# Kernel tuning notes

Measured on AMD Instinct MI355X. Metric: run time of the kernel, lower is better.

Reference implementation:

```python
import jax, jax.numpy as jnp
import numpy as np

B, T, C, H = 8, 1024, 768, 12
HD = C // H  # 64, even for RoPE
ROPE_THETA = 10000.0


def precompute_freqs_cis(dim, end, theta=ROPE_THETA):
    # [end, dim//2, 2] with (cos, sin) in last axis
    freqs = 1.0 / theta ** (jnp.arange(0, dim // 2).astype(jnp.float32) / (dim // 2))
    t = jnp.arange(end)
    f = jnp.outer(t, freqs)
    return jnp.stack([jnp.cos(f), jnp.sin(f)], axis=-1)


def apply_rope(x, fc):
    # x: [B,T,H,hd]; fc: [T,1,hd//2,2] (broadcasts over B and H)
    xr = x.reshape(*x.shape[:-1], -1, 2)
    x_re, x_im = xr[..., 0], xr[..., 1]
    cos, sin = fc[..., 0], fc[..., 1]
    out_re = x_re * cos - x_im * sin
    out_im = x_re * sin + x_im * cos
    return jnp.stack([out_re, out_im], axis=-1).reshape(x.shape)


def setup_inputs() -> dict:
    key = jax.random.key(0)
    k0, k1, k2 = jax.random.split(key, 3)
    x = jax.random.normal(k0, (B, T, C), jnp.float32)
    Wqkv = jax.random.normal(k1, (C, 3 * C), jnp.float32) * 0.02
    bqkv = jnp.zeros((3 * C,), jnp.float32)
    Wproj = jax.random.normal(k2, (C, C), jnp.float32) * 0.02
    bproj = jnp.zeros((C,), jnp.float32)
    mask = jnp.tril(jnp.ones((T, T), jnp.int32))  # causal
    return {"x": x, "Wqkv": Wqkv, "bqkv": bqkv, "Wproj": Wproj, "bproj": bproj, "mask": mask}


def reference(x, Wqkv, bqkv, Wproj, bproj, mask):
    B_, T_, C_ = x.shape
    qkv = (x @ Wqkv + bqkv).reshape(B_, T_, 3, H, HD)
    q, k, v = qkv[:, :, 0], qkv[:, :, 1], qkv[:, :, 2]  # each [B,T,H,hd]
    fc = precompute_freqs_cis(HD, T_)[:, None]  # [T,1,hd//2,2]
    q = apply_rope(q, fc)
    k = apply_rope(k, fc)
    scale = 1.0 / jnp.sqrt(jnp.float32(HD))
    attn = jnp.einsum('bthd,bkhd->bhtk', q, k) * scale  # [B,H,T,T]
    neg = jnp.finfo(attn.dtype).min
    attn = jnp.where(mask[None, None, :, :] == 0, neg, attn)
    attn = jax.nn.softmax(attn, axis=-1)
    out = jnp.einsum('bhtk,bkhd->bthd', attn, v).reshape(B_, T_, C_)
    return out @ Wproj + bproj
```

## Files before the change

kernel.cpp:

```cpp
#include <hip/hip_runtime.h>
#include <cstdint>
#include <cstddef>

#define BB 8
#define TT 1024
#define CC 768
#define NH 12
#define HD 64

using bf16x8 = __attribute__((ext_vector_type(8))) short;
using f32x4  = __attribute__((ext_vector_type(4))) float;

static __device__ __forceinline__ short f2bf(float f) {
    uint32_t u;
    __builtin_memcpy(&u, &f, 4);
    u += 0x7FFFu + ((u >> 16) & 1u);
    return (short)(u >> 16);
}

static __device__ __forceinline__ uint32_t bfpack(float lo, float hi) {
    return (uint32_t)(uint16_t)f2bf(lo) | ((uint32_t)(uint16_t)f2bf(hi) << 16);
}

__global__ void fc_kernel(float2* __restrict__ fc) {
    int idx = blockIdx.x * 256 + threadIdx.x;
    int t = idx >> 5, p = idx & 31;
    float freq = powf(10000.0f, -(float)p / 32.0f);
    float a = (float)t * freq;
    fc[idx] = make_float2(cosf(a), sinf(a));
}

__global__ __launch_bounds__(256)
void transpose_cast_kernel(const float* __restrict__ in, short* __restrict__ out,
                           int R, int Cdim) {
    __shared__ float tile[32][33];
    int tx = threadIdx.x, ty = threadIdx.y;
    int c0 = blockIdx.x * 32, r0 = blockIdx.y * 32;
#pragma unroll
    for (int i = 0; i < 4; i++)
        tile[ty + 8 * i][tx] = in[(size_t)(r0 + ty + 8 * i) * Cdim + c0 + tx];
    __syncthreads();
#pragma unroll
    for (int i = 0; i < 4; i++)
        out[(size_t)(c0 + ty + 8 * i) * R + r0 + tx] = f2bf(tile[tx][ty + 8 * i]);
}

__global__ __launch_bounds__(256)
void vtrans_kernel(const short* __restrict__ V, short* __restrict__ VT) {
    __shared__ short tl[64][72];
    const int tid = threadIdx.x;
    const int bh = blockIdx.y, t0 = blockIdx.x * 64;
    {
        int r = tid >> 2, cs = (tid & 3) * 16;
        const short* src = V + (size_t)bh * TT * HD + (size_t)(t0 + r) * HD + cs;
        *(bf16x8*)&tl[r][cs]     = *(const bf16x8*)src;
        *(bf16x8*)&tl[r][cs + 8] = *(const bf16x8*)(src + 8);
    }
    __syncthreads();
    {
        int d = tid >> 2, ts = (tid & 3) * 16;
        bf16x8 o0, o1;
#pragma unroll
        for (int e = 0; e < 8; e++) { o0[e] = tl[ts + e][d]; o1[e] = tl[ts + 8 + e][d]; }
        short* dst = VT + (size_t)bh * TT * HD + (size_t)d * TT + t0 + ts;
        *(bf16x8*)dst       = o0;
        *(bf16x8*)(dst + 8) = o1;
    }
}

template <bool AF32, int EPI>
__global__ __launch_bounds__(256)
void gemm_kernel(const void* __restrict__ Av, const short* __restrict__ BT,
                 const float* __restrict__ bias, int Kdim,
                 short* __restrict__ Qb, short* __restrict__ Kb, short* __restrict__ Vb,
                 const float2* __restrict__ fc, float* __restrict__ out) {
    __shared__ short As[128 * 64];
    __shared__ short Bs[128 * 64];
    const int tid = threadIdx.x;
    const int lane = tid & 63, wid = tid >> 6;
    const int g = lane >> 4, c = lane & 15;
    const int wm = wid >> 1, wn = wid & 1;
    const int m0 = blockIdx.y * 128, n0 = blockIdx.x * 128;

    const f32x4 zero4 = {0.f, 0.f, 0.f, 0.f};
    f32x4 acc[4][4];
#pragma unroll
    for (int i = 0; i < 4; i++)
#pragma unroll
        for (int j = 0; j < 4; j++) acc[i][j] = zero4;

    const int row_s = tid >> 3;
    const int kg = tid & 7;

    for (int k0 = 0; k0 < Kdim; k0 += 64) {
        if (AF32) {
            const float* Ap = (const float*)Av;
#pragma unroll
            for (int i = 0; i < 4; i++) {
                int row = row_s + 32 * i;
                const float* src = Ap + (size_t)(m0 + row) * Kdim + k0 + kg * 8;
                float4 f0 = *(const float4*)src;
                float4 f1 = *(const float4*)(src + 4);
                bf16x8 hv;
                hv[0] = f2bf(f0.x); hv[1] = f2bf(f0.y); hv[2] = f2bf(f0.z); hv[3] = f2bf(f0.w);
                hv[4] = f2bf(f1.x); hv[5] = f2bf(f1.y); hv[6] = f2bf(f1.z); hv[7] = f2bf(f1.w);
                *(bf16x8*)(&As[row * 64 + ((kg ^ (row & 7)) * 8)]) = hv;
            }
        } else {
            const short* Ap = (const short*)Av;
#pragma unroll
            for (int i = 0; i < 4; i++) {
                int row = row_s + 32 * i;
                bf16x8 hv = *(const bf16x8*)(Ap + (size_t)(m0 + row) * Kdim + k0 + kg * 8);
                *(bf16x8*)(&As[row * 64 + ((kg ^ (row & 7)) * 8)]) = hv;
            }
        }
#pragma unroll
        for (int i = 0; i < 4; i++) {
            int row = row_s + 32 * i;
            bf16x8 hv = *(const bf16x8*)(BT + (size_t)(n0 + row) * Kdim + k0 + kg * 8);
            *(bf16x8*)(&Bs[row * 64 + ((kg ^ (row & 7)) * 8)]) = hv;
        }
        __syncthreads();
#pragma unroll
        for (int kk = 0; kk < 2; kk++) {
            bf16x8 af[4], bfr[4];
#pragma unroll
            for (int mi = 0; mi < 4; mi++) {
                int row = wm * 64 + mi * 16 + c;
                af[mi] = *(const bf16x8*)(&As[row * 64 + (((kk * 4 + g) ^ (c & 7)) * 8)]);
            }
#pragma unroll
            for (int ni = 0; ni < 4; ni++) {
                int row = wn * 64 + ni * 16 + c;
                bfr[ni] = *(const bf16x8*)(&Bs[row * 64 + (((kk * 4 + g) ^ (c & 7)) * 8)]);
            }
#pragma unroll
            for (int mi = 0; mi < 4; mi++)
#pragma unroll
                for (int ni = 0; ni < 4; ni++)
                    acc[mi][ni] = __builtin_amdgcn_mfma_f32_16x16x32_bf16(
                        af[mi], bfr[ni], acc[mi][ni], 0, 0, 0);
        }
        __syncthreads();
    }

#pragma unroll
    for (int mi = 0; mi < 4; mi++) {
#pragma unroll
        for (int ni = 0; ni < 4; ni++) {
            int n = n0 + wn * 64 + ni * 16 + c;
            float bv = bias[n];
#pragma unroll
            for (int r = 0; r < 4; r++) {
                int m = m0 + wm * 64 + mi * 16 + g * 4 + r;
                float v = acc[mi][ni][r] + bv;
                if (EPI == 0) {
                    float pv = __shfl_xor(v, 1);
                    int part = (n >= 1536) ? 2 : (n >= 768 ? 1 : 0);
                    int rem = n - part * 768;
                    int h = rem >> 6, d = rem & 63;
                    int b = m >> 10, t = m & 1023;
                    if (part < 2) {
                        float2 cs = fc[t * 32 + (d >> 1)];
                        v = (d & 1) ? (pv * cs.y + v * cs.x) : (v * cs.x - pv * cs.y);
                        if (part == 0) v *= 0.125f;
                    }
                    size_t idx = (((size_t)b * NH + h) * TT + t) * HD + d;
                    (part == 0 ? Qb : part == 1 ? Kb : Vb)[idx] = f2bf(v);
                } else {
                    out[(size_t)m * CC + n] = v;
                }
            }
        }
    }
}

__global__ __launch_bounds__(256)
void attn_kernel(const short* __restrict__ Qb, const short* __restrict__ Kb,
                 const short* __restrict__ VT, short* __restrict__ Ob) {
    __shared__ uint32_t Pt[4][32][32];
    __shared__ uint32_t ot[128 * 32];
    const int tid = threadIdx.x, lane = tid & 63, wid = tid >> 6;
    const int g = lane >> 4, c = lane & 15;
    const int bh = blockIdx.x, qb = 7 - (int)blockIdx.y;
    const int b = bh / NH, h = bh % NH;
    const short* Qp = Qb + (size_t)bh * TT * HD;
    const short* Kp = Kb + (size_t)bh * TT * HD;
    const short* Vp = VT + (size_t)bh * TT * HD;
    const int q0 = qb * 128 + wid * 32;
    const int sw = (c & 7) << 2;

    bf16x8 qf[2][2];
#pragma unroll
    for (int qs = 0; qs < 2; qs++)
#pragma unroll
        for (int kh = 0; kh < 2; kh++)
            qf[qs][kh] = *(const bf16x8*)(Qp + (size_t)(q0 + qs * 16 + c) * HD + kh * 32 + g * 8);

    const f32x4 zero4 = {0.f, 0.f, 0.f, 0.f};
    f32x4 o[2][4];
#pragma unroll
    for (int qs = 0; qs < 2; qs++)
#pragma unroll
        for (int dt = 0; dt < 4; dt++) o[qs][dt] = zero4;
    float mrun[2] = {-1e30f, -1e30f}, lrun[2] = {0.f, 0.f};

    const int t0max = ((q0 + 31) >> 6) << 6;
    for (int t0 = 0; t0 <= t0max; t0 += 64) {
        f32x4 st[2][4];
#pragma unroll
        for (int nt = 0; nt < 4; nt++) {
            const short* kp = Kp + (size_t)(t0 + nt * 16 + c) * HD + g * 8;
            bf16x8 k0 = *(const bf16x8*)kp;
            bf16x8 k1 = *(const bf16x8*)(kp + 32);
#pragma unroll
            for (int qs = 0; qs < 2; qs++) {
                f32x4 z = zero4;
                z = __builtin_amdgcn_mfma_f32_16x16x32_bf16(k0, qf[qs][0], z, 0, 0, 0);
                z = __builtin_amdgcn_mfma_f32_16x16x32_bf16(k1, qf[qs][1], z, 0, 0, 0);
                st[qs][nt] = z;
            }
        }
        bf16x8 vf[2][4];
#pragma unroll
        for (int blk = 0; blk < 2; blk++)
#pragma unroll
            for (int dt = 0; dt < 4; dt++)
                vf[blk][dt] = *(const bf16x8*)(Vp + (size_t)(dt * 16 + c) * TT + t0 + blk * 32 + g * 8);
        if (t0 + 63 > q0) {
#pragma unroll
            for (int qs = 0; qs < 2; qs++) {
                int q = q0 + qs * 16 + c;
#pragma unroll
                for (int nt = 0; nt < 4; nt++)
#pragma unroll
                    for (int r = 0; r < 4; r++)
                        if (t0 + nt * 16 + g * 4 + r > q) st[qs][nt][r] = -1e30f;
            }
        }
#pragma unroll
        for (int qs = 0; qs < 2; qs++) {
            float mx = st[qs][0][0];
#pragma unroll
            for (int nt = 0; nt < 4; nt++)
#pragma unroll
                for (int r = 0; r < 4; r++) mx = fmaxf(mx, st[qs][nt][r]);
            mx = fmaxf(mx, __shfl_xor(mx, 16));
            mx = fmaxf(mx, __shfl_xor(mx, 32));
            float mnew = fmaxf(mrun[qs], mx);
            float al = __expf(mrun[qs] - mnew);
            mrun[qs] = mnew;
            float sm = 0.f;
#pragma unroll
            for (int nt = 0; nt < 4; nt++)
#pragma unroll
                for (int r = 0; r < 4; r++) {
                    float e = __expf(st[qs][nt][r] - mnew);
                    st[qs][nt][r] = e;
                    sm += e;
                }
            sm += __shfl_xor(sm, 16);
            sm += __shfl_xor(sm, 32);
            lrun[qs] = lrun[qs] * al + sm;
#pragma unroll
            for (int dt = 0; dt < 4; dt++) {
                o[qs][dt][0] *= al; o[qs][dt][1] *= al;
                o[qs][dt][2] *= al; o[qs][dt][3] *= al;
            }
            int row = qs * 16 + c;
#pragma unroll
            for (int nt = 0; nt < 4; nt++) {
                uint32_t w0 = bfpack(st[qs][nt][0], st[qs][nt][1]);
                uint32_t w1 = bfpack(st[qs][nt][2], st[qs][nt][3]);
                int wa = nt * 8 + 2 * g;
                Pt[wid][row][wa ^ sw]       = w0;
                Pt[wid][row][(wa + 1) ^ sw] = w1;
            }
        }
#pragma unroll
        for (int qs = 0; qs < 2; qs++) {
            int row = qs * 16 + c;
#pragma unroll
            for (int blk = 0; blk < 2; blk++) {
                bf16x8 pf = *(const bf16x8*)&Pt[wid][row][(blk * 16 + 4 * g) ^ sw];
#pragma unroll
                for (int dt = 0; dt < 4; dt++)
                    o[qs][dt] = __builtin_amdgcn_mfma_f32_16x16x32_bf16(
                        vf[blk][dt], pf, o[qs][dt], 0, 0, 0);
            }
        }
    }

#pragma unroll
    for (int qs = 0; qs < 2; qs++) {
        float inv = 1.0f / lrun[qs];
        int ql = wid * 32 + qs * 16 + c;
#pragma unroll
        for (int dt = 0; dt < 4; dt++) {
            uint32_t w0 = bfpack(o[qs][dt][0] * inv, o[qs][dt][1] * inv);
            uint32_t w1 = bfpack(o[qs][dt][2] * inv, o[qs][dt][3] * inv);
            int jc0 = dt * 8 + 2 * g;
            int jc1 = jc0 + 1;
            ot[ql * 32 + ((((jc0 >> 2) ^ (c & 7)) << 2) | (jc0 & 3))] = w0;
            ot[ql * 32 + ((((jc1 >> 2) ^ (c & 7)) << 2) | (jc1 & 3))] = w1;
        }
    }
    __syncthreads();
#pragma unroll
    for (int p = 0; p < 4; p++) {
        int q = (tid >> 3) + 32 * p;
        int jb = tid & 7;
        const uint32_t* src = &ot[q * 32 + ((jb ^ (q & 7)) << 2)];
        int4 w = *(const int4*)src;
        *(int4*)(Ob + ((size_t)b * TT + qb * 128 + q) * CC + h * HD + jb * 8) = w;
    }
}

extern "C" void kernel_launch(void* const* d_in, const int* in_sizes, int n_in,
                              void* d_out, int out_size, void* d_ws, size_t ws_size,
                              hipStream_t stream) {
    const float* x     = (const float*)d_in[0];
    const float* Wqkv  = (const float*)d_in[1];
    const float* bqkv  = (const float*)d_in[2];
    const float* Wproj = (const float*)d_in[3];
    const float* bproj = (const float*)d_in[4];

    char* ws = (char*)d_ws;
    short*  WqkvT  = (short*)(ws);
    short*  WprojT = (short*)(ws + 3538944);
    float2* fc     = (float2*)(ws + 3538944 + 1179648);
    short*  Qb     = (short*)(ws + 4980736);
    short*  Kb     = (short*)(ws + 4980736 + 1 * 12582912);
    short*  VOb    = (short*)(ws + 4980736 + 2 * 12582912);
    short*  VbT    = (short*)(ws + 4980736 + 3 * 12582912);
    float*  out    = (float*)d_out;

    hipLaunchKernelGGL(fc_kernel, dim3(128), dim3(256), 0, stream, fc);
    hipLaunchKernelGGL(transpose_cast_kernel, dim3(72, 24), dim3(32, 8), 0, stream,
                       Wqkv, WqkvT, 768, 2304);
    hipLaunchKernelGGL(transpose_cast_kernel, dim3(24, 24), dim3(32, 8), 0, stream,
                       Wproj, WprojT, 768, 768);
    hipLaunchKernelGGL((gemm_kernel<true, 0>), dim3(18, 64), dim3(256), 0, stream,
                       (const void*)x, WqkvT, bqkv, 768, Qb, Kb, VOb, fc, (float*)nullptr);
    hipLaunchKernelGGL(vtrans_kernel, dim3(16, 96), dim3(256), 0, stream, VOb, VbT);
    hipLaunchKernelGGL(attn_kernel, dim3(96, 8), dim3(256), 0, stream, Qb, Kb, VbT, VOb);
    hipLaunchKernelGGL((gemm_kernel<false, 1>), dim3(6, 64), dim3(256), 0, stream,
                       (const void*)VOb, WprojT, bproj, 768,
                       (short*)nullptr, (short*)nullptr, (short*)nullptr,
                       (const float2*)nullptr, out);
}
```

Measured before the change: 195.2 us.

## Use direct global-to-LDS loads in GEMM, pre-cast x, stage QKV epilogue

Adds a separate kernel that casts x to bf16 up front, so the GEMM always takes bf16 A operands. The GEMM tile loads now use global_load_lds (16-byte direct-to-LDS), which drops the XOR swizzle and the register round-trip. Blocks are remapped in an XCD-aware order for better L2 locality. The QKV epilogue packs RoPE'd pairs into LDS and writes 16-byte vectorized rows to Q/K/V instead of scattered 2-byte stores. The trade-offs are an extra launch plus the bf16 x round-trip through memory, and possible LDS bank conflicts now that the swizzle on fragment reads is gone.

```diff
diff --git a/kernel.cpp b/kernel.cpp
--- a/kernel.cpp
+++ b/kernel.cpp
@@ -21,6 +21,11 @@
 static __device__ __forceinline__ uint32_t bfpack(float lo, float hi) {
     return (uint32_t)(uint16_t)f2bf(lo) | ((uint32_t)(uint16_t)f2bf(hi) << 16);
 }
+
+#define GLOAD_LDS16(gp, lp)                                                        \
+    __builtin_amdgcn_global_load_lds(                                              \
+        (const __attribute__((address_space(1))) void*)(gp),                       \
+        (__attribute__((address_space(3))) void*)(lp), 16, 0, 0)
 
 __global__ void fc_kernel(float2* __restrict__ fc) {
     int idx = blockIdx.x * 256 + threadIdx.x;
@@ -28,6 +33,17 @@
     float freq = powf(10000.0f, -(float)p / 32.0f);
     float a = (float)t * freq;
     fc[idx] = make_float2(cosf(a), sinf(a));
+}
+
+__global__ __launch_bounds__(256)
+void cast_kernel(const float* __restrict__ in, short* __restrict__ out) {
+    int i = (blockIdx.x * 256 + threadIdx.x) * 8;
+    float4 f0 = *(const float4*)(in + i);
+    float4 f1 = *(const float4*)(in + i + 4);
+    bf16x8 h;
+    h[0] = f2bf(f0.x); h[1] = f2bf(f0.y); h[2] = f2bf(f0.z); h[3] = f2bf(f0.w);
+    h[4] = f2bf(f1.x); h[5] = f2bf(f1.y); h[6] = f2bf(f1.z); h[7] = f2bf(f1.w);
+    *(bf16x8*)(out + i) = h;
 }
 
 __global__ __launch_bounds__(256)
@@ -68,19 +84,24 @@
     }
 }
 
-template <bool AF32, int EPI>
-__global__ __launch_bounds__(256)
-void gemm_kernel(const void* __restrict__ Av, const short* __restrict__ BT,
-                 const float* __restrict__ bias, int Kdim,
+template <int EPI>
+__global__ __launch_bounds__(256)
+void gemm_kernel(const short* __restrict__ Agl, const short* __restrict__ BT,
+                 const float* __restrict__ bias,
                  short* __restrict__ Qb, short* __restrict__ Kb, short* __restrict__ Vb,
                  const float2* __restrict__ fc, float* __restrict__ out) {
-    __shared__ short As[128 * 64];
-    __shared__ short Bs[128 * 64];
+    __shared__ __align__(16) char smem[32768];
+    short* As = (short*)smem;
+    short* Bs = (short*)(smem + 16384);
     const int tid = threadIdx.x;
     const int lane = tid & 63, wid = tid >> 6;
     const int g = lane >> 4, c = lane & 15;
     const int wm = wid >> 1, wn = wid & 1;
-    const int m0 = blockIdx.y * 128, n0 = blockIdx.x * 128;
+
+    const int bid = blockIdx.y * gridDim.x + blockIdx.x;
+    const int cpx = (gridDim.x * gridDim.y) >> 3;
+    const int swz = (bid & 7) * cpx + (bid >> 3);
+    const int m0 = (swz / gridDim.x) * 128, n0 = (swz % gridDim.x) * 128;
 
     const f32x4 zero4 = {0.f, 0.f, 0.f, 0.f};
     f32x4 acc[4][4];
@@ -89,52 +110,27 @@
 #pragma unroll
         for (int j = 0; j < 4; j++) acc[i][j] = zero4;
 
-    const int row_s = tid >> 3;
-    const int kg = tid & 7;
-
-    for (int k0 = 0; k0 < Kdim; k0 += 64) {
-        if (AF32) {
-            const float* Ap = (const float*)Av;
-#pragma unroll
-            for (int i = 0; i < 4; i++) {
-                int row = row_s + 32 * i;
-                const float* src = Ap + (size_t)(m0 + row) * Kdim + k0 + kg * 8;
-                float4 f0 = *(const float4*)src;
-                float4 f1 = *(const float4*)(src + 4);
-                bf16x8 hv;
-                hv[0] = f2bf(f0.x); hv[1] = f2bf(f0.y); hv[2] = f2bf(f0.z); hv[3] = f2bf(f0.w);
-                hv[4] = f2bf(f1.x); hv[5] = f2bf(f1.y); hv[6] = f2bf(f1.z); hv[7] = f2bf(f1.w);
-                *(bf16x8*)(&As[row * 64 + ((kg ^ (row & 7)) * 8)]) = hv;
-            }
-        } else {
-            const short* Ap = (const short*)Av;
-#pragma unroll
-            for (int i = 0; i < 4; i++) {
-                int row = row_s + 32 * i;
-                bf16x8 hv = *(const bf16x8*)(Ap + (size_t)(m0 + row) * Kdim + k0 + kg * 8);
-                *(bf16x8*)(&As[row * 64 + ((kg ^ (row & 7)) * 8)]) = hv;
-            }
-        }
-#pragma unroll
-        for (int i = 0; i < 4; i++) {
-            int row = row_s + 32 * i;
-            bf16x8 hv = *(const bf16x8*)(BT + (size_t)(n0 + row) * Kdim + k0 + kg * 8);
-            *(bf16x8*)(&Bs[row * 64 + ((kg ^ (row & 7)) * 8)]) = hv;
+    const int rowb = lane >> 3;
+    const int colb = (lane & 7) * 8;
+
+    for (int k0 = 0; k0 < 768; k0 += 64) {
+        const short* ga = Agl + (size_t)(m0 + wid * 32 + rowb) * 768 + k0 + colb;
+        const short* gb = BT  + (size_t)(n0 + wid * 32 + rowb) * 768 + k0 + colb;
+#pragma unroll
+        for (int q = 0; q < 4; q++) {
+            GLOAD_LDS16(ga + (size_t)q * 8 * 768, As + (wid * 32 + q * 8) * 64);
+            GLOAD_LDS16(gb + (size_t)q * 8 * 768, Bs + (wid * 32 + q * 8) * 64);
         }
         __syncthreads();
 #pragma unroll
         for (int kk = 0; kk < 2; kk++) {
             bf16x8 af[4], bfr[4];
 #pragma unroll
-            for (int mi = 0; mi < 4; mi++) {
-                int row = wm * 64 + mi * 16 + c;
-                af[mi] = *(const bf16x8*)(&As[row * 64 + (((kk * 4 + g) ^ (c & 7)) * 8)]);
-            }
-#pragma unroll
-            for (int ni = 0; ni < 4; ni++) {
-                int row = wn * 64 + ni * 16 + c;
-                bfr[ni] = *(const bf16x8*)(&Bs[row * 64 + (((kk * 4 + g) ^ (c & 7)) * 8)]);
-            }
+            for (int mi = 0; mi < 4; mi++)
+                af[mi] = *(const bf16x8*)&As[(wm * 64 + mi * 16 + c) * 64 + kk * 32 + g * 8];
+#pragma unroll
+            for (int ni = 0; ni < 4; ni++)
+                bfr[ni] = *(const bf16x8*)&Bs[(wn * 64 + ni * 16 + c) * 64 + kk * 32 + g * 8];
 #pragma unroll
             for (int mi = 0; mi < 4; mi++)
 #pragma unroll
@@ -145,34 +141,64 @@
         __syncthreads();
     }
 
-#pragma unroll
-    for (int mi = 0; mi < 4; mi++) {
+    if (EPI == 0) {
+        uint32_t* LD = (uint32_t*)smem;
 #pragma unroll
         for (int ni = 0; ni < 4; ni++) {
-            int n = n0 + wn * 64 + ni * 16 + c;
+            int nl = wn * 64 + ni * 16 + c;
+            int n = n0 + nl;
             float bv = bias[n];
-#pragma unroll
-            for (int r = 0; r < 4; r++) {
-                int m = m0 + wm * 64 + mi * 16 + g * 4 + r;
-                float v = acc[mi][ni][r] + bv;
-                if (EPI == 0) {
+            int part = (n >= 1536) ? 2 : (n >= 768 ? 1 : 0);
+            int d = (n - part * 768) & 63;
+#pragma unroll
+            for (int mi = 0; mi < 4; mi++) {
+#pragma unroll
+                for (int r = 0; r < 4; r++) {
+                    int ml = wm * 64 + mi * 16 + g * 4 + r;
+                    float v = acc[mi][ni][r] + bv;
                     float pv = __shfl_xor(v, 1);
-                    int part = (n >= 1536) ? 2 : (n >= 768 ? 1 : 0);
-                    int rem = n - part * 768;
-                    int h = rem >> 6, d = rem & 63;
-                    int b = m >> 10, t = m & 1023;
-                    if (part < 2) {
-                        float2 cs = fc[t * 32 + (d >> 1)];
-                        v = (d & 1) ? (pv * cs.y + v * cs.x) : (v * cs.x - pv * cs.y);
-                        if (part == 0) v *= 0.125f;
+                    if (!(c & 1)) {
+                        float o0, o1;
+                        if (part < 2) {
+                            int t = (m0 + ml) & 1023;
+                            float2 cs = fc[t * 32 + (d >> 1)];
+                            o0 = v * cs.x - pv * cs.y;
+                            o1 = v * cs.y + pv * cs.x;
+                            if (part == 0) { o0 *= 0.125f; o1 *= 0.125f; }
+                        } else { o0 = v; o1 = pv; }
+                        LD[ml * 64 + ((nl >> 1) ^ (((ml >> 2) & 3) << 3))] = bfpack(o0, o1);
                     }
-                    size_t idx = (((size_t)b * NH + h) * TT + t) * HD + d;
-                    (part == 0 ? Qb : part == 1 ? Kb : Vb)[idx] = f2bf(v);
-                } else {
-                    out[(size_t)m * CC + n] = v;
                 }
             }
         }
+        __syncthreads();
+#pragma unroll
+        for (int p = 0; p < 8; p++) {
+            int ml = p * 16 + (tid >> 4);
+            int wc = (tid & 15) * 4;
+            int4 dat = *(const int4*)&LD[ml * 64 + (wc ^ (((ml >> 2) & 3) << 3))];
+            int n = n0 + wc * 2;
+            int part = (n >= 1536) ? 2 : (n >= 768 ? 1 : 0);
+            int rem = n - part * 768;
+            int h = rem >> 6, d = rem & 63;
+            int m = m0 + ml, b = m >> 10, t = m & 1023;
+            short* dst = (part == 0 ? Qb : part == 1 ? Kb : Vb)
+                         + (((size_t)b * NH + h) * TT + t) * HD + d;
+            *(int4*)dst = dat;
+        }
+    } else {
+#pragma unroll
+        for (int mi = 0; mi < 4; mi++)
+#pragma unroll
+            for (int ni = 0; ni < 4; ni++) {
+                int n = n0 + wn * 64 + ni * 16 + c;
+                float bv = bias[n];
+#pragma unroll
+                for (int r = 0; r < 4; r++) {
+                    int m = m0 + wm * 64 + mi * 16 + g * 4 + r;
+                    out[(size_t)m * CC + n] = acc[mi][ni][r] + bv;
+                }
+            }
     }
 }
 
@@ -334,6 +360,7 @@
     short*  Kb     = (short*)(ws + 4980736 + 1 * 12582912);
     short*  VOb    = (short*)(ws + 4980736 + 2 * 12582912);
     short*  VbT    = (short*)(ws + 4980736 + 3 * 12582912);
+    short*  xb     = VbT;
     float*  out    = (float*)d_out;
 
     hipLaunchKernelGGL(fc_kernel, dim3(128), dim3(256), 0, stream, fc);
@@ -341,12 +368,13 @@
                        Wqkv, WqkvT, 768, 2304);
     hipLaunchKernelGGL(transpose_cast_kernel, dim3(24, 24), dim3(32, 8), 0, stream,
                        Wproj, WprojT, 768, 768);
-    hipLaunchKernelGGL((gemm_kernel<true, 0>), dim3(18, 64), dim3(256), 0, stream,
-                       (const void*)x, WqkvT, bqkv, 768, Qb, Kb, VOb, fc, (float*)nullptr);
+    hipLaunchKernelGGL(cast_kernel, dim3(3072), dim3(256), 0, stream, x, xb);
+    hipLaunchKernelGGL((gemm_kernel<0>), dim3(18, 64), dim3(256), 0, stream,
+                       xb, WqkvT, bqkv, Qb, Kb, VOb, fc, (float*)nullptr);
     hipLaunchKernelGGL(vtrans_kernel, dim3(16, 96), dim3(256), 0, stream, VOb, VbT);
     hipLaunchKernelGGL(attn_kernel, dim3(96, 8), dim3(256), 0, stream, Qb, Kb, VbT, VOb);
-    hipLaunchKernelGGL((gemm_kernel<false, 1>), dim3(6, 64), dim3(256), 0, stream,
-                       (const void*)VOb, WprojT, bproj, 768,
+    hipLaunchKernelGGL((gemm_kernel<1>), dim3(6, 64), dim3(256), 0, stream,
+                       VOb, WprojT, bproj,
                        (short*)nullptr, (short*)nullptr, (short*)nullptr,
                        (const float2*)nullptr, out);
 }
```

Result: no change. 192.3 us (-1.5%).
